# Optimization experiments

Hardware: AMD Instinct MI355X
Metric: run time of the kernel (lower is better)

Reference implementation:

```python
import jax, jax.numpy as jnp
import numpy as np

C = 1.0          # ball curvature magnitude (manifold.c)
EPS = 1e-5       # boundary projection epsilon
MIN_NORM = 1e-15

def _norm(x):
    return jnp.maximum(jnp.linalg.norm(x, axis=-1, keepdims=True), MIN_NORM)

def artanh(x):
    return jnp.arctanh(jnp.clip(x, -1.0 + 1e-7, 1.0 - 1e-7))

def proj(x, c=C):
    # clip points to the open Poincare ball of radius 1/sqrt(c)
    n = _norm(x)
    maxnorm = (1.0 - EPS) / jnp.sqrt(c)
    return jnp.where(n > maxnorm, x / n * maxnorm, x)

def logmap0(x, c=C):
    sc = jnp.sqrt(c)
    n = _norm(x)
    return artanh(sc * n) * x / (sc * n)

def expmap0(u, c=C):
    sc = jnp.sqrt(c)
    n = _norm(u)
    return jnp.tanh(sc * n) * u / (sc * n)

def gyro_add(x, y, c=C):
    # Mobius (gyrovector) addition
    x2 = jnp.sum(x * x, -1, keepdims=True)
    y2 = jnp.sum(y * y, -1, keepdims=True)
    xy = jnp.sum(x * y, -1, keepdims=True)
    num = (1.0 + 2.0 * c * xy + c * y2) * x + (1.0 - c * x2) * y
    den = 1.0 + 2.0 * c * xy + c * c * x2 * y2
    return num / jnp.maximum(den, MIN_NORM)

def gyro_matvec(W, x, c=C):
    # Mobius matrix-vector multiplication (pv_gyro_matvec)
    sc = jnp.sqrt(c)
    xn = _norm(x)
    mx = x @ W.T                       # [N, out]
    mxn = _norm(mx)
    res = jnp.tanh(mxn / xn * artanh(sc * xn)) * mx / (mxn * sc)
    zero = jnp.all(mx == 0.0, axis=-1, keepdims=True)
    return jnp.where(zero, jnp.zeros_like(res), res)

def hyp_linear(x, W, b, c=C):
    # CustomHyperbolicLinear (activation=None branch): mobius matvec + hyp bias gyro-add
    res = proj(gyro_matvec(W, x, c), c)
    hyp_bias = proj(expmap0(b[None, :], c), c)   # proj_tan0 is identity on the ball
    res = proj(gyro_add(res, hyp_bias, c), c)
    return res

def hyp_tanh_act(x, c=C):
    # CustomHyperbolicActivation(manifold, nn.Tanh()): tanh in tangent space at origin
    x = proj(x, c)
    t = jnp.tanh(logmap0(x, c))
    return proj(expmap0(t, c), c)


def setup_inputs() -> dict:
    key = jax.random.key(0)
    k0, k1, k2 = jax.random.split(key, 3)
    N, D, H = 32768, 1024, 1024
    x = proj(0.1 * jax.random.normal(k0, (N, D), dtype=jnp.float32))
    gain = float(np.sqrt(2.0))
    bound1 = gain * float(np.sqrt(6.0 / (D + H)))   # xavier_uniform with gain sqrt(2)
    W1 = jax.random.uniform(k1, (H, D), jnp.float32, -bound1, bound1)
    b1 = jnp.zeros((H,), jnp.float32)
    bound2 = gain * float(np.sqrt(6.0 / (H + H)))
    W2 = jax.random.uniform(k2, (H, H), jnp.float32, -bound2, bound2)
    b2 = jnp.zeros((H,), jnp.float32)
    return {"x": x, "W1": W1, "b1": b1, "W2": W2, "b2": b2}


def reference(x, W1, b1, W2, b2):
    # GeometricModel forward: two CustomHyperbolicLayer blocks
    # (hyperbolic linear -> tangent-space tanh activation)
    h = hyp_linear(x, W1, b1)
    h = hyp_tanh_act(h)
    h = hyp_linear(h, W2, b2)
    h = hyp_tanh_act(h)
    return h
```

## Files before the change

### kernel.cpp

```cpp
#include <hip/hip_runtime.h>


typedef short short8 __attribute__((ext_vector_type(8)));
typedef unsigned short u16x8 __attribute__((ext_vector_type(8)));
typedef unsigned short u16x4 __attribute__((ext_vector_type(4)));
typedef float f32x4 __attribute__((ext_vector_type(4)));

#define MAXN (1.0f - 1e-5f)

__device__ __forceinline__ float bf2f(unsigned short u) {
    return __uint_as_float(((unsigned int)u) << 16);
}
__device__ __forceinline__ unsigned short f2bf(float f) {
    unsigned int u = __float_as_uint(f);
    u += 0x7FFFu + ((u >> 16) & 1u);
    return (unsigned short)(u >> 16);
}
__device__ __forceinline__ float wave_sum(float v) {
#pragma unroll
    for (int m = 32; m > 0; m >>= 1) v += __shfl_xor(v, m, 64);
    return v;
}
__device__ __forceinline__ float tanh_fast(float x) {
    float e = __expf(2.0f * x);
    return 1.0f - __fdividef(2.0f, e + 1.0f);
}
__device__ __forceinline__ float artanh_clip(float x) {
    x = fminf(fmaxf(x, -1.0f + 1e-7f), 1.0f - 1e-7f);
    return 0.5f * __logf(__fdividef(1.0f + x, 1.0f - x));
}

__device__ __forceinline__ void gld_lds16(const unsigned short* g, unsigned short* l) {
    __builtin_amdgcn_global_load_lds(
        (const __attribute__((address_space(1))) unsigned int*)g,
        (__attribute__((address_space(3))) unsigned int*)l,
        16, 0, 0);
}

__global__ __launch_bounds__(256) void cast_x_kernel(
    const float* __restrict__ X, unsigned short* __restrict__ Xb,
    float* __restrict__ xn, int K)
{
    int row = blockIdx.x * 4 + (threadIdx.x >> 6);
    int l = threadIdx.x & 63;
    const float4* xr = (const float4*)(X + (size_t)row * K);
    u16x4* xw = (u16x4*)(Xb + (size_t)row * K);
    float ss = 0.f;
#pragma unroll
    for (int i = 0; i < 4; ++i) {
        float4 v = xr[i * 64 + l];
        ss += v.x * v.x + v.y * v.y + v.z * v.z + v.w * v.w;
        u16x4 o;
        o[0] = f2bf(v.x); o[1] = f2bf(v.y); o[2] = f2bf(v.z); o[3] = f2bf(v.w);
        xw[i * 64 + l] = o;
    }
    ss = wave_sum(ss);
    if (l == 0) xn[row] = fmaxf(sqrtf(ss), 1e-15f);
}

__global__ __launch_bounds__(256) void cast_w_kernel(
    const float* __restrict__ W1, unsigned short* __restrict__ W1b,
    const float* __restrict__ W2, unsigned short* __restrict__ W2b, int n4each)
{
    int i = blockIdx.x * 256 + threadIdx.x;
    const float4* src;
    u16x4* dst;
    if (i < n4each) { src = (const float4*)W1; dst = (u16x4*)W1b; }
    else            { src = (const float4*)W2; dst = (u16x4*)W2b; i -= n4each; }
    float4 v = src[i];
    u16x4 o;
    o[0] = f2bf(v.x); o[1] = f2bf(v.y); o[2] = f2bf(v.z); o[3] = f2bf(v.w);
    dst[i] = o;
}

#define STAGE(rs_, kt_) do {                                            \
    const int ko_ = (kt_) << 5;                                         \
    gld_lds16(Ab + ga0 + ko_, &sA[(rs_) * 8192 + c0 * 8]);              \
    gld_lds16(Ab + ga1 + ko_, &sA[(rs_) * 8192 + c1 * 8]);              \
    gld_lds16(Bb + ga0 + ko_, &sB[(rs_) * 8192 + c0 * 8]);              \
    gld_lds16(Bb + ga1 + ko_, &sB[(rs_) * 8192 + c1 * 8]);              \
} while (0)

#define LDFRAG(FA_, FB_, kt_) do {                                                  \
    const int rb_ = ((kt_) & 3) * 8192;                                             \
    const unsigned short* pa_ = &sA[rb_ + (wm + lr) * 32 + swo];                    \
    const unsigned short* pb_ = &sB[rb_ + (wn + lr) * 32 + swo];                    \
    _Pragma("unroll")                                                               \
    for (int m_ = 0; m_ < 8; ++m_) FA_[m_] = *(const short8*)(pa_ + m_ * 512);      \
    _Pragma("unroll")                                                               \
    for (int n_ = 0; n_ < 4; ++n_) FB_[n_] = *(const short8*)(pb_ + n_ * 512);      \
} while (0)

#define MFMAB(FA_, FB_)                                                             \
    _Pragma("unroll")                                                               \
    for (int m_ = 0; m_ < 8; ++m_)                                                  \
        _Pragma("unroll")                                                           \
        for (int n_ = 0; n_ < 4; ++n_)                                              \
            acc[m_][n_] = __builtin_amdgcn_mfma_f32_16x16x32_bf16(                  \
                FA_[m_], FB_[n_], acc[m_][n_], 0, 0, 0);

#define PSTEP(kt_, FAC_, FBC_, FAN_, FBN_, DOSTAGE_, DOPF_, DOVM_, VMSTR_, DOBAR_) {\
    if (DOSTAGE_) { STAGE((((kt_) + 3) & 3), (kt_) + 3); }                          \
    if (DOPF_) { LDFRAG(FAN_, FBN_, (kt_) + 1); }                                   \
    __builtin_amdgcn_s_setprio(1);                                                  \
    MFMAB(FAC_, FBC_);                                                              \
    __builtin_amdgcn_s_setprio(0);                                                  \
    if (DOVM_) { asm volatile("s_waitcnt vmcnt(" VMSTR_ ")" ::: "memory"); }        \
    if (DOBAR_) { __builtin_amdgcn_s_barrier(); }                                   \
}

__global__ __launch_bounds__(512, 2) void gemm_bt_kernel(
    const unsigned short* __restrict__ A,
    const unsigned short* __restrict__ B,
    unsigned short* __restrict__ C,
    int M, int Nc, int K)
{
    __shared__ __align__(16) unsigned short sA[4 * 256 * 32];
    __shared__ __align__(16) unsigned short sB[4 * 256 * 32];

    const int t = threadIdx.x;
    const int l = t & 63;
    const int w = t >> 6;
    const int lr = l & 15;
    const int lq = l >> 4;

    const int nwg = gridDim.x;
    const int cpx = nwg >> 3;
    const int swz = (blockIdx.x & 7) * cpx + (blockIdx.x >> 3);
    const int nb = Nc >> 8;
    const int bm = swz / nb;
    const int bn = swz % nb;

    const unsigned short* Ab = A + (size_t)bm * 256 * K;
    const unsigned short* Bb = B + (size_t)bn * 256 * K;

    const int wm = (w >> 2) * 128;
    const int wn = (w & 3) * 64;

    const int c0 = t, c1 = t + 512;
    const int r0 = c0 >> 2, s0 = (c0 & 3) ^ ((r0 >> 1) & 3);
    const int r1 = c1 >> 2, s1 = (c1 & 3) ^ ((r1 >> 1) & 3);
    const size_t ga0 = (size_t)r0 * K + s0 * 8;
    const size_t ga1 = (size_t)r1 * K + s1 * 8;

    const int swo = (lq ^ ((lr >> 1) & 3)) * 8;

    f32x4 acc[8][4];
#pragma unroll
    for (int i = 0; i < 8; ++i)
#pragma unroll
        for (int j = 0; j < 4; ++j)
            acc[i][j] = (f32x4){0.f, 0.f, 0.f, 0.f};

    STAGE(0, 0);
    STAGE(1, 1);
    STAGE(2, 2);
    asm volatile("s_waitcnt vmcnt(4)" ::: "memory");
    __builtin_amdgcn_s_barrier();

    short8 fa0[8], fb0[4], fa1[8], fb1[4];
    LDFRAG(fa0, fb0, 0);

    const int NTK = K >> 5;
    int kt = 0;
#pragma unroll 1
    for (; kt < NTK - 4; kt += 2) {
        PSTEP(kt,     fa0, fb0, fa1, fb1, true, true, true, "4", true);
        PSTEP(kt + 1, fa1, fb1, fa0, fb0, true, true, true, "4", true);
    }
    PSTEP(NTK - 4, fa0, fb0, fa1, fb1, true,  true,  true,  "4", true);
    PSTEP(NTK - 3, fa1, fb1, fa0, fb0, false, true,  true,  "0", true);
    PSTEP(NTK - 2, fa0, fb0, fa1, fb1, false, true,  false, "0", false);
    PSTEP(NTK - 1, fa1, fb1, fa0, fb0, false, false, false, "0", false);

    unsigned short* Cb = C + (size_t)(bm * 256 + wm) * Nc + bn * 256 + wn;
#pragma unroll
    for (int i = 0; i < 8; ++i)
#pragma unroll
        for (int r = 0; r < 4; ++r) {
            unsigned short* Cr = Cb + (size_t)(i * 16 + lq * 4 + r) * Nc + lr;
#pragma unroll
            for (int j = 0; j < 4; ++j)
                Cr[j * 16] = f2bf(acc[i][j][r]);
        }
}

template <int OUTF32>
__global__ __launch_bounds__(256) void hyp_epilogue_kernel(
    const unsigned short* __restrict__ mx, const float* __restrict__ xn_in,
    const float* __restrict__ bvec, void* __restrict__ outp,
    float* __restrict__ xn_out, int H)
{
    int row = blockIdx.x * 4 + (threadIdx.x >> 6);
    int l = threadIdx.x & 63;
    const u16x8* mrow = (const u16x8*)(mx + (size_t)row * H);
    u16x8 mv0 = mrow[l], mv1 = mrow[64 + l];
    const float4* bf4 = (const float4*)bvec;
    float4 bq0 = bf4[l * 2], bq1 = bf4[l * 2 + 1];
    float4 bq2 = bf4[128 + l * 2], bq3 = bf4[128 + l * 2 + 1];

    float m[16], b[16];
#pragma unroll
    for (int i = 0; i < 8; ++i) { m[i] = bf2f(mv0[i]); m[8 + i] = bf2f(mv1[i]); }
    b[0] = bq0.x; b[1] = bq0.y; b[2] = bq0.z; b[3] = bq0.w;
    b[4] = bq1.x; b[5] = bq1.y; b[6] = bq1.z; b[7] = bq1.w;
    b[8] = bq2.x; b[9] = bq2.y; b[10] = bq2.z; b[11] = bq2.w;
    b[12] = bq3.x; b[13] = bq3.y; b[14] = bq3.z; b[15] = bq3.w;

    float ssm = 0.f, ssb = 0.f, dmb = 0.f;
#pragma unroll
    for (int i = 0; i < 16; ++i) {
        ssm += m[i] * m[i]; ssb += b[i] * b[i]; dmb += m[i] * b[i];
    }
    ssm = wave_sum(ssm); ssb = wave_sum(ssb); dmb = wave_sum(dmb);

    float mxn = fmaxf(sqrtf(ssm), 1e-15f);
    float bn  = fmaxf(sqrtf(ssb), 1e-15f);
    float xn  = xn_in[row];

    float tt = tanh_fast(__fdividef(mxn, xn) * artanh_clip(xn));
    float rnorm = fabsf(tt);
    float pr = (rnorm > MAXN) ? __fdividef(MAXN, rnorm) : 1.0f;
    float resScale = __fdividef(tt * pr, mxn);
    float rn = fminf(rnorm, MAXN);
    float x2 = rn * rn;

    float tb = tanh_fast(bn);
    float hbn = fabsf(tb);
    float pb = (hbn > MAXN) ? __fdividef(MAXN, hbn) : 1.0f;
    float hscale = __fdividef(tb, bn) * pb;
    float hn = fminf(hbn, MAXN);
    float y2 = hn * hn;

    float xy = resScale * hscale * dmb;
    float ca = 1.0f + 2.0f * xy + y2;
    float cb = 1.0f - x2;
    float den = fmaxf(1.0f + 2.0f * xy + x2 * y2, 1e-15f);
    float fA = __fdividef(ca * resScale, den);
    float fB = __fdividef(cb * hscale, den);

    float ssz = fA * fA * ssm + 2.0f * fA * fB * dmb + fB * fB * ssb;
    float zn = fmaxf(sqrtf(fmaxf(ssz, 0.0f)), 1e-15f);
    float pz = (zn > MAXN) ? __fdividef(MAXN, zn) : 1.0f;
    float n2 = fmaxf(fminf(zn, MAXN), 1e-15f);
    float g = __fdividef(artanh_clip(n2), n2) * pz;

    float u[16];
    float ssu = 0.f;
#pragma unroll
    for (int i = 0; i < 16; ++i) {
        float zi = fA * m[i] + fB * b[i];
        u[i] = tanh_fast(g * zi);
        ssu += u[i] * u[i];
    }
    ssu = wave_sum(ssu);
    float un = fmaxf(sqrtf(ssu), 1e-15f);
    float te = tanh_fast(un);
    float on = fabsf(te);
    float po = (on > MAXN) ? __fdividef(MAXN, on) : 1.0f;
    float os = __fdividef(te, un) * po;

    if (OUTF32) {
        float* of = (float*)outp + (size_t)row * H;
        float4* of4 = (float4*)of;
        float4 a0, a1, a2, a3;
        a0.x = os * u[0];  a0.y = os * u[1];  a0.z = os * u[2];  a0.w = os * u[3];
        a1.x = os * u[4];  a1.y = os * u[5];  a1.z = os * u[6];  a1.w = os * u[7];
        a2.x = os * u[8];  a2.y = os * u[9];  a2.z = os * u[10]; a2.w = os * u[11];
        a3.x = os * u[12]; a3.y = os * u[13]; a3.z = os * u[14]; a3.w = os * u[15];
        of4[l * 2] = a0; of4[l * 2 + 1] = a1;
        of4[128 + l * 2] = a2; of4[128 + l * 2 + 1] = a3;
    } else {
        u16x8 o0, o1;
#pragma unroll
        for (int i = 0; i < 8; ++i) { o0[i] = f2bf(os * u[i]); o1[i] = f2bf(os * u[8 + i]); }
        u16x8* orow = (u16x8*)((unsigned short*)outp + (size_t)row * H);
        orow[l] = o0; orow[64 + l] = o1;
    }
    if (l == 0) xn_out[row] = fmaxf(fminf(on, MAXN), 1e-15f);
}

extern "C" void kernel_launch(void* const* d_in, const int* in_sizes, int n_in,
                              void* d_out, int out_size, void* d_ws, size_t ws_size,
                              hipStream_t stream)
{
    const float* x  = (const float*)d_in[0];
    const float* W1 = (const float*)d_in[1];
    const float* b1 = (const float*)d_in[2];
    const float* W2 = (const float*)d_in[3];
    const float* b2 = (const float*)d_in[4];

    const int H = in_sizes[2];
    const int D = in_sizes[1] / H;
    const int N = in_sizes[0] / D;

    unsigned short* stage = (unsigned short*)d_out;
    float* outf = (float*)d_out;

    unsigned short* mxb = (unsigned short*)d_ws;
    unsigned short* W1b = mxb + (size_t)N * H;
    unsigned short* W2b = W1b + (size_t)H * D;
    float* xn1 = (float*)(W2b + (size_t)H * H);
    float* xn2 = xn1 + N;

    dim3 blk(256);
    dim3 gblk(512);
    const int gemm_grid = (N / 256) * (H / 256);
    const int n4w = H * D / 4;

    cast_x_kernel<<<N / 4, blk, 0, stream>>>(x, stage, xn1, D);
    cast_w_kernel<<<(2 * n4w + 255) / 256, blk, 0, stream>>>(W1, W1b, W2, W2b, n4w);
    gemm_bt_kernel<<<gemm_grid, gblk, 0, stream>>>(stage, W1b, mxb, N, H, D);
    hyp_epilogue_kernel<0><<<N / 4, blk, 0, stream>>>(mxb, xn1, b1, stage, xn2, H);
    gemm_bt_kernel<<<gemm_grid, gblk, 0, stream>>>(stage, W2b, mxb, N, H, H);
    hyp_epilogue_kernel<1><<<N / 4, blk, 0, stream>>>(mxb, xn2, b2, outf, xn1, H);
}
```

Before: 470.1 us.

## Shrink GEMM tile to 128x128 with 3-slot LDS ring and 256-thread blocks

The bf16 GEMM drops from 256x256 tiles with 512 threads and a 4-deep LDS ring to 128x128 tiles with 256 threads, a 3-slot LDS ring and launch bounds allowing 3 blocks per CU. The main loop is unrolled by 6 to cycle the ring slots statically, and an lgkmcnt wait now precedes each barrier. The aim is more resident blocks and better latency hiding across many more workgroups. In exchange each tile reuses its global loads less, so memory traffic per flop rises.

Result: slower. 487.2 us (+3.6%).

```diff
diff --git a/kernel.cpp b/kernel.cpp
--- a/kernel.cpp
+++ b/kernel.cpp
@@ -73,50 +73,54 @@
     dst[i] = o;
 }
 
-#define STAGE(rs_, kt_) do {                                            \
+#define VMC(n_) asm volatile("s_waitcnt vmcnt(" #n_ ")" ::: "memory")
+
+#define STAGE3(slot_, kt_) do {                                         \
     const int ko_ = (kt_) << 5;                                         \
-    gld_lds16(Ab + ga0 + ko_, &sA[(rs_) * 8192 + c0 * 8]);              \
-    gld_lds16(Ab + ga1 + ko_, &sA[(rs_) * 8192 + c1 * 8]);              \
-    gld_lds16(Bb + ga0 + ko_, &sB[(rs_) * 8192 + c0 * 8]);              \
-    gld_lds16(Bb + ga1 + ko_, &sB[(rs_) * 8192 + c1 * 8]);              \
+    gld_lds16(Ab + ga0 + ko_, &sA[(slot_) * 4096 + c0 * 8]);            \
+    gld_lds16(Ab + ga1 + ko_, &sA[(slot_) * 4096 + c1 * 8]);            \
+    gld_lds16(Bb + ga0 + ko_, &sB[(slot_) * 4096 + c0 * 8]);            \
+    gld_lds16(Bb + ga1 + ko_, &sB[(slot_) * 4096 + c1 * 8]);            \
 } while (0)
 
-#define LDFRAG(FA_, FB_, kt_) do {                                                  \
-    const int rb_ = ((kt_) & 3) * 8192;                                             \
-    const unsigned short* pa_ = &sA[rb_ + (wm + lr) * 32 + swo];                    \
-    const unsigned short* pb_ = &sB[rb_ + (wn + lr) * 32 + swo];                    \
+#define LDFRAG3(FA_, FB_, slot_) do {                                               \
+    const unsigned short* pa_ = &sA[(slot_) * 4096 + (wm + lr) * 32 + swo];         \
+    const unsigned short* pb_ = &sB[(slot_) * 4096 + (wn + lr) * 32 + swo];         \
     _Pragma("unroll")                                                               \
-    for (int m_ = 0; m_ < 8; ++m_) FA_[m_] = *(const short8*)(pa_ + m_ * 512);      \
+    for (int m_ = 0; m_ < 4; ++m_) FA_[m_] = *(const short8*)(pa_ + m_ * 512);      \
     _Pragma("unroll")                                                               \
     for (int n_ = 0; n_ < 4; ++n_) FB_[n_] = *(const short8*)(pb_ + n_ * 512);      \
 } while (0)
 
-#define MFMAB(FA_, FB_)                                                             \
+#define MFMAB3(FA_, FB_)                                                            \
     _Pragma("unroll")                                                               \
-    for (int m_ = 0; m_ < 8; ++m_)                                                  \
+    for (int m_ = 0; m_ < 4; ++m_)                                                  \
         _Pragma("unroll")                                                           \
         for (int n_ = 0; n_ < 4; ++n_)                                              \
             acc[m_][n_] = __builtin_amdgcn_mfma_f32_16x16x32_bf16(                  \
                 FA_[m_], FB_[n_], acc[m_][n_], 0, 0, 0);
 
-#define PSTEP(kt_, FAC_, FBC_, FAN_, FBN_, DOSTAGE_, DOPF_, DOVM_, VMSTR_, DOBAR_) {\
-    if (DOSTAGE_) { STAGE((((kt_) + 3) & 3), (kt_) + 3); }                          \
-    if (DOPF_) { LDFRAG(FAN_, FBN_, (kt_) + 1); }                                   \
+#define PS3(KT_, SLST_, SLPF_, FAC_, FBC_, FAN_, FBN_, DOST_, DOPF_, DOVM_, VMS_, DOBAR_) { \
+    if (DOST_) { STAGE3(SLST_, (KT_) + 3); }                                        \
+    if (DOPF_) { LDFRAG3(FAN_, FBN_, SLPF_); }                                      \
     __builtin_amdgcn_s_setprio(1);                                                  \
-    MFMAB(FAC_, FBC_);                                                              \
+    MFMAB3(FAC_, FBC_);                                                             \
     __builtin_amdgcn_s_setprio(0);                                                  \
-    if (DOVM_) { asm volatile("s_waitcnt vmcnt(" VMSTR_ ")" ::: "memory"); }        \
-    if (DOBAR_) { __builtin_amdgcn_s_barrier(); }                                   \
-}
-
-__global__ __launch_bounds__(512, 2) void gemm_bt_kernel(
+    if (DOVM_) { asm volatile("s_waitcnt vmcnt(" VMS_ ")" ::: "memory"); }          \
+    if (DOBAR_) {                                                                   \
+        asm volatile("s_waitcnt lgkmcnt(0)" ::: "memory");                          \
+        __builtin_amdgcn_s_barrier();                                               \
+    }                                                                               \
+}
+
+__global__ __launch_bounds__(256, 3) void gemm_bt_kernel(
     const unsigned short* __restrict__ A,
     const unsigned short* __restrict__ B,
     unsigned short* __restrict__ C,
     int M, int Nc, int K)
 {
-    __shared__ __align__(16) unsigned short sA[4 * 256 * 32];
-    __shared__ __align__(16) unsigned short sB[4 * 256 * 32];
+    __shared__ __align__(16) unsigned short sA[3 * 128 * 32];
+    __shared__ __align__(16) unsigned short sB[3 * 128 * 32];
 
     const int t = threadIdx.x;
     const int l = t & 63;
@@ -127,17 +131,17 @@
     const int nwg = gridDim.x;
     const int cpx = nwg >> 3;
     const int swz = (blockIdx.x & 7) * cpx + (blockIdx.x >> 3);
-    const int nb = Nc >> 8;
+    const int nb = Nc >> 7;
     const int bm = swz / nb;
     const int bn = swz % nb;
 
-    const unsigned short* Ab = A + (size_t)bm * 256 * K;
-    const unsigned short* Bb = B + (size_t)bn * 256 * K;
-
-    const int wm = (w >> 2) * 128;
-    const int wn = (w & 3) * 64;
-
-    const int c0 = t, c1 = t + 512;
+    const unsigned short* Ab = A + (size_t)bm * 128 * K;
+    const unsigned short* Bb = B + (size_t)bn * 128 * K;
+
+    const int wm = (w >> 1) * 64;
+    const int wn = (w & 1) * 64;
+
+    const int c0 = t, c1 = t + 256;
     const int r0 = c0 >> 2, s0 = (c0 & 3) ^ ((r0 >> 1) & 3);
     const int r1 = c1 >> 2, s1 = (c1 & 3) ^ ((r1 >> 1) & 3);
     const size_t ga0 = (size_t)r0 * K + s0 * 8;
@@ -145,37 +149,47 @@
 
     const int swo = (lq ^ ((lr >> 1) & 3)) * 8;
 
-    f32x4 acc[8][4];
-#pragma unroll
-    for (int i = 0; i < 8; ++i)
+    f32x4 acc[4][4];
+#pragma unroll
+    for (int i = 0; i < 4; ++i)
 #pragma unroll
         for (int j = 0; j < 4; ++j)
             acc[i][j] = (f32x4){0.f, 0.f, 0.f, 0.f};
 
-    STAGE(0, 0);
-    STAGE(1, 1);
-    STAGE(2, 2);
-    asm volatile("s_waitcnt vmcnt(4)" ::: "memory");
+    STAGE3(0, 0);
+    STAGE3(1, 1);
+    STAGE3(2, 2);
+    VMC(4);
     __builtin_amdgcn_s_barrier();
 
-    short8 fa0[8], fb0[4], fa1[8], fb1[4];
-    LDFRAG(fa0, fb0, 0);
+    short8 fa0[4], fb0[4], fa1[4], fb1[4];
+    LDFRAG3(fa0, fb0, 0);
+    asm volatile("s_waitcnt lgkmcnt(0)" ::: "memory");
+    __builtin_amdgcn_s_barrier();
 
     const int NTK = K >> 5;
     int kt = 0;
 #pragma unroll 1
-    for (; kt < NTK - 4; kt += 2) {
-        PSTEP(kt,     fa0, fb0, fa1, fb1, true, true, true, "4", true);
-        PSTEP(kt + 1, fa1, fb1, fa0, fb0, true, true, true, "4", true);
-    }
-    PSTEP(NTK - 4, fa0, fb0, fa1, fb1, true,  true,  true,  "4", true);
-    PSTEP(NTK - 3, fa1, fb1, fa0, fb0, false, true,  true,  "0", true);
-    PSTEP(NTK - 2, fa0, fb0, fa1, fb1, false, true,  false, "0", false);
-    PSTEP(NTK - 1, fa1, fb1, fa0, fb0, false, false, false, "0", false);
-
-    unsigned short* Cb = C + (size_t)(bm * 256 + wm) * Nc + bn * 256 + wn;
-#pragma unroll
-    for (int i = 0; i < 8; ++i)
+    for (; kt < NTK - 8; kt += 6) {
+        PS3(kt,     0, 1, fa0, fb0, fa1, fb1, 1, 1, 1, "4", 1);
+        PS3(kt + 1, 1, 2, fa1, fb1, fa0, fb0, 1, 1, 1, "4", 1);
+        PS3(kt + 2, 2, 0, fa0, fb0, fa1, fb1, 1, 1, 1, "4", 1);
+        PS3(kt + 3, 0, 1, fa1, fb1, fa0, fb0, 1, 1, 1, "4", 1);
+        PS3(kt + 4, 1, 2, fa0, fb0, fa1, fb1, 1, 1, 1, "4", 1);
+        PS3(kt + 5, 2, 0, fa1, fb1, fa0, fb0, 1, 1, 1, "4", 1);
+    }
+    PS3(NTK - 8, 0, 1, fa0, fb0, fa1, fb1, 1, 1, 1, "4", 1);
+    PS3(NTK - 7, 1, 2, fa1, fb1, fa0, fb0, 1, 1, 1, "4", 1);
+    PS3(NTK - 6, 2, 0, fa0, fb0, fa1, fb1, 1, 1, 1, "4", 1);
+    PS3(NTK - 5, 0, 1, fa1, fb1, fa0, fb0, 1, 1, 1, "4", 1);
+    PS3(NTK - 4, 1, 2, fa0, fb0, fa1, fb1, 1, 1, 1, "4", 1);
+    PS3(NTK - 3, 2, 0, fa1, fb1, fa0, fb0, 0, 1, 1, "0", 1);
+    PS3(NTK - 2, 0, 1, fa0, fb0, fa1, fb1, 0, 1, 0, "0", 0);
+    PS3(NTK - 1, 0, 0, fa1, fb1, fa0, fb0, 0, 0, 0, "0", 0);
+
+    unsigned short* Cb = C + (size_t)(bm * 128 + wm) * Nc + bn * 128 + wn;
+#pragma unroll
+    for (int i = 0; i < 4; ++i)
 #pragma unroll
         for (int r = 0; r < 4; ++r) {
             unsigned short* Cr = Cb + (size_t)(i * 16 + lq * 4 + r) * Nc + lr;
@@ -304,14 +318,13 @@
     float* xn2 = xn1 + N;
 
     dim3 blk(256);
-    dim3 gblk(512);
-    const int gemm_grid = (N / 256) * (H / 256);
+    const int gemm_grid = (N / 128) * (H / 128);
     const int n4w = H * D / 4;
 
     cast_x_kernel<<<N / 4, blk, 0, stream>>>(x, stage, xn1, D);
     cast_w_kernel<<<(2 * n4w + 255) / 256, blk, 0, stream>>>(W1, W1b, W2, W2b, n4w);
-    gemm_bt_kernel<<<gemm_grid, gblk, 0, stream>>>(stage, W1b, mxb, N, H, D);
+    gemm_bt_kernel<<<gemm_grid, blk, 0, stream>>>(stage, W1b, mxb, N, H, D);
     hyp_epilogue_kernel<0><<<N / 4, blk, 0, stream>>>(mxb, xn1, b1, stage, xn2, H);
-    gemm_bt_kernel<<<gemm_grid, gblk, 0, stream>>>(stage, W2b, mxb, N, H, H);
+    gemm_bt_kernel<<<gemm_grid, blk, 0, stream>>>(stage, W2b, mxb, N, H, H);
     hyp_epilogue_kernel<1><<<N / 4, blk, 0, stream>>>(mxb, xn2, b2, outf, xn1, H);
 }
```

## Fuse x cast, GEMM and hyperbolic epilogue into one full-row layer kernel

Applied to the files above, without the earlier changes.

Replaces the separate cast, 256x256-tile GEMM and row epilogue kernels with one kernel per layer. Each block owns 64 full output rows across all 1024 columns, so row norms and dot products can be reduced in-block and the bf16 intermediate mx never goes to global memory. The first layer also converts x to bf16 and computes its norm while staging. In exchange the tile is narrow (64 rows), the pipeline drops from 4-stage to 2-stage double buffering with a full wait every step, and occupancy is one block per CU with a large LDS footprint. Together these may lower MFMA efficiency relative to the earlier tuned GEMM.

After: 507.3 us. 1.08x slower.

```diff
diff --git a/kernel.cpp b/kernel.cpp
--- a/kernel.cpp
+++ b/kernel.cpp
@@ -35,27 +35,6 @@
         (const __attribute__((address_space(1))) unsigned int*)g,
         (__attribute__((address_space(3))) unsigned int*)l,
         16, 0, 0);
-}
-
-__global__ __launch_bounds__(256) void cast_x_kernel(
-    const float* __restrict__ X, unsigned short* __restrict__ Xb,
-    float* __restrict__ xn, int K)
-{
-    int row = blockIdx.x * 4 + (threadIdx.x >> 6);
-    int l = threadIdx.x & 63;
-    const float4* xr = (const float4*)(X + (size_t)row * K);
-    u16x4* xw = (u16x4*)(Xb + (size_t)row * K);
-    float ss = 0.f;
-#pragma unroll
-    for (int i = 0; i < 4; ++i) {
-        float4 v = xr[i * 64 + l];
-        ss += v.x * v.x + v.y * v.y + v.z * v.z + v.w * v.w;
-        u16x4 o;
-        o[0] = f2bf(v.x); o[1] = f2bf(v.y); o[2] = f2bf(v.z); o[3] = f2bf(v.w);
-        xw[i * 64 + l] = o;
-    }
-    ss = wave_sum(ss);
-    if (l == 0) xn[row] = fmaxf(sqrtf(ss), 1e-15f);
 }
 
 __global__ __launch_bounds__(256) void cast_w_kernel(
@@ -73,150 +52,163 @@
     dst[i] = o;
 }
 
-#define STAGE(rs_, kt_) do {                                            \
-    const int ko_ = (kt_) << 5;                                         \
-    gld_lds16(Ab + ga0 + ko_, &sA[(rs_) * 8192 + c0 * 8]);              \
-    gld_lds16(Ab + ga1 + ko_, &sA[(rs_) * 8192 + c1 * 8]);              \
-    gld_lds16(Bb + ga0 + ko_, &sB[(rs_) * 8192 + c0 * 8]);              \
-    gld_lds16(Bb + ga1 + ko_, &sB[(rs_) * 8192 + c1 * 8]);              \
-} while (0)
-
-#define LDFRAG(FA_, FB_, kt_) do {                                                  \
-    const int rb_ = ((kt_) & 3) * 8192;                                             \
-    const unsigned short* pa_ = &sA[rb_ + (wm + lr) * 32 + swo];                    \
-    const unsigned short* pb_ = &sB[rb_ + (wn + lr) * 32 + swo];                    \
-    _Pragma("unroll")                                                               \
-    for (int m_ = 0; m_ < 8; ++m_) FA_[m_] = *(const short8*)(pa_ + m_ * 512);      \
-    _Pragma("unroll")                                                               \
-    for (int n_ = 0; n_ < 4; ++n_) FB_[n_] = *(const short8*)(pb_ + n_ * 512);      \
-} while (0)
-
-#define MFMAB(FA_, FB_)                                                             \
-    _Pragma("unroll")                                                               \
-    for (int m_ = 0; m_ < 8; ++m_)                                                  \
-        _Pragma("unroll")                                                           \
-        for (int n_ = 0; n_ < 4; ++n_)                                              \
-            acc[m_][n_] = __builtin_amdgcn_mfma_f32_16x16x32_bf16(                  \
-                FA_[m_], FB_[n_], acc[m_][n_], 0, 0, 0);
-
-#define PSTEP(kt_, FAC_, FBC_, FAN_, FBN_, DOSTAGE_, DOPF_, DOVM_, VMSTR_, DOBAR_) {\
-    if (DOSTAGE_) { STAGE((((kt_) + 3) & 3), (kt_) + 3); }                          \
-    if (DOPF_) { LDFRAG(FAN_, FBN_, (kt_) + 1); }                                   \
-    __builtin_amdgcn_s_setprio(1);                                                  \
-    MFMAB(FAC_, FBC_);                                                              \
-    __builtin_amdgcn_s_setprio(0);                                                  \
-    if (DOVM_) { asm volatile("s_waitcnt vmcnt(" VMSTR_ ")" ::: "memory"); }        \
-    if (DOBAR_) { __builtin_amdgcn_s_barrier(); }                                   \
-}
-
-__global__ __launch_bounds__(512, 2) void gemm_bt_kernel(
-    const unsigned short* __restrict__ A,
+template <int FIRST>
+__global__ __launch_bounds__(512, 1) void fused_layer_kernel(
+    const float* __restrict__ Af,
+    const unsigned short* __restrict__ Ah,
     const unsigned short* __restrict__ B,
-    unsigned short* __restrict__ C,
-    int M, int Nc, int K)
+    const float* __restrict__ bvec,
+    const float* __restrict__ xn_in,
+    void* __restrict__ outp,
+    float* __restrict__ xn_out,
+    int K, int Nc)
 {
-    __shared__ __align__(16) unsigned short sA[4 * 256 * 32];
-    __shared__ __align__(16) unsigned short sB[4 * 256 * 32];
+    __shared__ __align__(16) unsigned short sB[2][1024 * 32];
+    __shared__ __align__(16) unsigned short sA[2][64 * 32];
+    __shared__ __align__(16) float sP1[64 * 8];
+    __shared__ __align__(16) float sP2[64 * 8];
+    __shared__ __align__(16) float sF[64 * 4];
+    __shared__ __align__(16) float sXN[64];
 
     const int t = threadIdx.x;
     const int l = t & 63;
     const int w = t >> 6;
     const int lr = l & 15;
     const int lq = l >> 4;
-
-    const int nwg = gridDim.x;
-    const int cpx = nwg >> 3;
-    const int swz = (blockIdx.x & 7) * cpx + (blockIdx.x >> 3);
-    const int nb = Nc >> 8;
-    const int bm = swz / nb;
-    const int bn = swz % nb;
-
-    const unsigned short* Ab = A + (size_t)bm * 256 * K;
-    const unsigned short* Bb = B + (size_t)bn * 256 * K;
-
-    const int wm = (w >> 2) * 128;
-    const int wn = (w & 3) * 64;
-
-    const int c0 = t, c1 = t + 512;
-    const int r0 = c0 >> 2, s0 = (c0 & 3) ^ ((r0 >> 1) & 3);
-    const int r1 = c1 >> 2, s1 = (c1 & 3) ^ ((r1 >> 1) & 3);
-    const size_t ga0 = (size_t)r0 * K + s0 * 8;
-    const size_t ga1 = (size_t)r1 * K + s1 * 8;
+    const int g0 = blockIdx.x * 64;
+    const int wn = w * 128;
+
+    size_t gaB[8];
+    int ldB[8];
+#pragma unroll
+    for (int j = 0; j < 8; ++j) {
+        int c = t + 512 * j;
+        int r = c >> 2, s = (c & 3) ^ ((r >> 1) & 3);
+        gaB[j] = (size_t)r * K + s * 8;
+        ldB[j] = c * 8;
+    }
+    const int rA = t >> 2;
+    const int sAs = (t & 3) ^ ((rA >> 1) & 3);
+    const size_t gaA = (size_t)(g0 + rA) * K + sAs * 8;
 
     const int swo = (lq ^ ((lr >> 1) & 3)) * 8;
 
-    f32x4 acc[8][4];
-#pragma unroll
-    for (int i = 0; i < 8; ++i)
-#pragma unroll
-        for (int j = 0; j < 4; ++j)
-            acc[i][j] = (f32x4){0.f, 0.f, 0.f, 0.f};
-
-    STAGE(0, 0);
-    STAGE(1, 1);
-    STAGE(2, 2);
-    asm volatile("s_waitcnt vmcnt(4)" ::: "memory");
+    f32x4 acc[4][8];
+#pragma unroll
+    for (int m = 0; m < 4; ++m)
+#pragma unroll
+        for (int n = 0; n < 8; ++n)
+            acc[m][n] = (f32x4){0.f, 0.f, 0.f, 0.f};
+
+    float ss = 0.f;
+
+    auto stage = [&](int buf, int kt) {
+#pragma unroll
+        for (int j = 0; j < 8; ++j)
+            gld_lds16(B + gaB[j] + kt * 32, &sB[buf][ldB[j]]);
+        if (t < 256) {
+            if constexpr (FIRST) {
+                float4 v0 = *(const float4*)(Af + gaA + kt * 32);
+                float4 v1 = *(const float4*)(Af + gaA + kt * 32 + 4);
+                ss += v0.x * v0.x + v0.y * v0.y + v0.z * v0.z + v0.w * v0.w;
+                ss += v1.x * v1.x + v1.y * v1.y + v1.z * v1.z + v1.w * v1.w;
+                u16x8 o;
+                o[0] = f2bf(v0.x); o[1] = f2bf(v0.y); o[2] = f2bf(v0.z); o[3] = f2bf(v0.w);
+                o[4] = f2bf(v1.x); o[5] = f2bf(v1.y); o[6] = f2bf(v1.z); o[7] = f2bf(v1.w);
+                *(u16x8*)&sA[buf][t * 8] = o;
+            } else {
+                gld_lds16(Ah + gaA + kt * 32, &sA[buf][t * 8]);
+            }
+        }
+    };
+
+    stage(0, 0);
+    asm volatile("s_waitcnt vmcnt(0) lgkmcnt(0)" ::: "memory");
     __builtin_amdgcn_s_barrier();
 
-    short8 fa0[8], fb0[4], fa1[8], fb1[4];
-    LDFRAG(fa0, fb0, 0);
-
     const int NTK = K >> 5;
-    int kt = 0;
 #pragma unroll 1
-    for (; kt < NTK - 4; kt += 2) {
-        PSTEP(kt,     fa0, fb0, fa1, fb1, true, true, true, "4", true);
-        PSTEP(kt + 1, fa1, fb1, fa0, fb0, true, true, true, "4", true);
-    }
-    PSTEP(NTK - 4, fa0, fb0, fa1, fb1, true,  true,  true,  "4", true);
-    PSTEP(NTK - 3, fa1, fb1, fa0, fb0, false, true,  true,  "0", true);
-    PSTEP(NTK - 2, fa0, fb0, fa1, fb1, false, true,  false, "0", false);
-    PSTEP(NTK - 1, fa1, fb1, fa0, fb0, false, false, false, "0", false);
-
-    unsigned short* Cb = C + (size_t)(bm * 256 + wm) * Nc + bn * 256 + wn;
-#pragma unroll
-    for (int i = 0; i < 8; ++i)
+    for (int kt = 0; kt < NTK; ++kt) {
+        const int buf = kt & 1;
+        if (kt + 1 < NTK) stage(buf ^ 1, kt + 1);
+        short8 a[4], b[8];
+#pragma unroll
+        for (int m = 0; m < 4; ++m)
+            a[m] = *(const short8*)&sA[buf][(m * 16 + lr) * 32 + swo];
+#pragma unroll
+        for (int n = 0; n < 8; ++n)
+            b[n] = *(const short8*)&sB[buf][(wn + n * 16 + lr) * 32 + swo];
+        __builtin_amdgcn_s_setprio(1);
+#pragma unroll
+        for (int m = 0; m < 4; ++m)
+#pragma unroll
+            for (int n = 0; n < 8; ++n)
+                acc[m][n] = __builtin_amdgcn_mfma_f32_16x16x32_bf16(a[m], b[n], acc[m][n], 0, 0, 0);
+        __builtin_amdgcn_s_setprio(0);
+        asm volatile("s_waitcnt vmcnt(0) lgkmcnt(0)" ::: "memory");
+        __builtin_amdgcn_s_barrier();
+    }
+
+
+    if constexpr (FIRST) {
+        if (t < 256) {
+            float s2 = ss;
+            s2 += __shfl_xor(s2, 1, 64);
+            s2 += __shfl_xor(s2, 2, 64);
+            if ((t & 3) == 0) sXN[t >> 2] = fmaxf(sqrtf(s2), 1e-15f);
+        }
+    }
+
+    float bn_[8];
+#pragma unroll
+    for (int n = 0; n < 8; ++n) bn_[n] = bvec[wn + n * 16 + lr];
+
+    float pm[4][4], pd[4][4];
+#pragma unroll
+    for (int m = 0; m < 4; ++m)
 #pragma unroll
         for (int r = 0; r < 4; ++r) {
-            unsigned short* Cr = Cb + (size_t)(i * 16 + lq * 4 + r) * Nc + lr;
-#pragma unroll
-            for (int j = 0; j < 4; ++j)
-                Cr[j * 16] = f2bf(acc[i][j][r]);
-        }
-}
-
-template <int OUTF32>
-__global__ __launch_bounds__(256) void hyp_epilogue_kernel(
-    const unsigned short* __restrict__ mx, const float* __restrict__ xn_in,
-    const float* __restrict__ bvec, void* __restrict__ outp,
-    float* __restrict__ xn_out, int H)
-{
-    int row = blockIdx.x * 4 + (threadIdx.x >> 6);
-    int l = threadIdx.x & 63;
-    const u16x8* mrow = (const u16x8*)(mx + (size_t)row * H);
-    u16x8 mv0 = mrow[l], mv1 = mrow[64 + l];
-    const float4* bf4 = (const float4*)bvec;
-    float4 bq0 = bf4[l * 2], bq1 = bf4[l * 2 + 1];
-    float4 bq2 = bf4[128 + l * 2], bq3 = bf4[128 + l * 2 + 1];
-
-    float m[16], b[16];
-#pragma unroll
-    for (int i = 0; i < 8; ++i) { m[i] = bf2f(mv0[i]); m[8 + i] = bf2f(mv1[i]); }
-    b[0] = bq0.x; b[1] = bq0.y; b[2] = bq0.z; b[3] = bq0.w;
-    b[4] = bq1.x; b[5] = bq1.y; b[6] = bq1.z; b[7] = bq1.w;
-    b[8] = bq2.x; b[9] = bq2.y; b[10] = bq2.z; b[11] = bq2.w;
-    b[12] = bq3.x; b[13] = bq3.y; b[14] = bq3.z; b[15] = bq3.w;
-
-    float ssm = 0.f, ssb = 0.f, dmb = 0.f;
-#pragma unroll
-    for (int i = 0; i < 16; ++i) {
-        ssm += m[i] * m[i]; ssb += b[i] * b[i]; dmb += m[i] * b[i];
-    }
-    ssm = wave_sum(ssm); ssb = wave_sum(ssb); dmb = wave_sum(dmb);
-
+            float sm = 0.f, sd = 0.f;
+#pragma unroll
+            for (int n = 0; n < 8; ++n) {
+                float v = acc[m][n][r];
+                sm += v * v;
+                sd += v * bn_[n];
+            }
+            pm[m][r] = sm; pd[m][r] = sd;
+        }
+#pragma unroll
+    for (int mask = 1; mask <= 8; mask <<= 1)
+#pragma unroll
+        for (int m = 0; m < 4; ++m)
+#pragma unroll
+            for (int r = 0; r < 4; ++r) {
+                pm[m][r] += __shfl_xor(pm[m][r], mask, 64);
+                pd[m][r] += __shfl_xor(pd[m][r], mask, 64);
+            }
+    if (lr == 0) {
+#pragma unroll
+        for (int m = 0; m < 4; ++m)
+#pragma unroll
+            for (int r = 0; r < 4; ++r) {
+                int row = m * 16 + lq * 4 + r;
+                sP1[row * 8 + w] = pm[m][r];
+                sP2[row * 8 + w] = pd[m][r];
+            }
+    }
+    __syncthreads();
+
+    float ssm = 0.f, dmb = 0.f;
+#pragma unroll
+    for (int j = 0; j < 8; ++j) { ssm += sP1[l * 8 + j]; dmb += sP2[l * 8 + j]; }
+    float ssb = 0.f;
+#pragma unroll
+    for (int j = 0; j < 16; ++j) { float bj = bvec[l + 64 * j]; ssb += bj * bj; }
+    ssb = wave_sum(ssb);
+
+    float xn = FIRST ? sXN[l] : fmaxf(xn_in[g0 + l], 1e-15f);
     float mxn = fmaxf(sqrtf(ssm), 1e-15f);
-    float bn  = fmaxf(sqrtf(ssb), 1e-15f);
-    float xn  = xn_in[row];
+    float bnn = fmaxf(sqrtf(ssb), 1e-15f);
 
     float tt = tanh_fast(__fdividef(mxn, xn) * artanh_clip(xn));
     float rnorm = fabsf(tt);
@@ -224,60 +216,94 @@
     float resScale = __fdividef(tt * pr, mxn);
     float rn = fminf(rnorm, MAXN);
     float x2 = rn * rn;
-
-    float tb = tanh_fast(bn);
+    float tb = tanh_fast(bnn);
     float hbn = fabsf(tb);
     float pb = (hbn > MAXN) ? __fdividef(MAXN, hbn) : 1.0f;
-    float hscale = __fdividef(tb, bn) * pb;
+    float hscale = __fdividef(tb, bnn) * pb;
     float hn = fminf(hbn, MAXN);
     float y2 = hn * hn;
-
     float xy = resScale * hscale * dmb;
     float ca = 1.0f + 2.0f * xy + y2;
     float cb = 1.0f - x2;
     float den = fmaxf(1.0f + 2.0f * xy + x2 * y2, 1e-15f);
     float fA = __fdividef(ca * resScale, den);
     float fB = __fdividef(cb * hscale, den);
-
     float ssz = fA * fA * ssm + 2.0f * fA * fB * dmb + fB * fB * ssb;
     float zn = fmaxf(sqrtf(fmaxf(ssz, 0.0f)), 1e-15f);
     float pz = (zn > MAXN) ? __fdividef(MAXN, zn) : 1.0f;
     float n2 = fmaxf(fminf(zn, MAXN), 1e-15f);
     float g = __fdividef(artanh_clip(n2), n2) * pz;
 
-    float u[16];
+    if (w == 0) {
+        float4 f4; f4.x = fA; f4.y = fB; f4.z = g; f4.w = 0.f;
+        *(float4*)&sF[l * 4] = f4;
+    }
+    __syncthreads();
+
+    float pu[4][4];
+#pragma unroll
+    for (int m = 0; m < 4; ++m)
+#pragma unroll
+        for (int r = 0; r < 4; ++r) {
+            int row = m * 16 + lq * 4 + r;
+            float4 f = *(const float4*)&sF[row * 4];
+            float su = 0.f;
+#pragma unroll
+            for (int n = 0; n < 8; ++n) {
+                float z = f.x * acc[m][n][r] + f.y * bn_[n];
+                float u = tanh_fast(f.z * z);
+                acc[m][n][r] = u;
+                su += u * u;
+            }
+            pu[m][r] = su;
+        }
+#pragma unroll
+    for (int mask = 1; mask <= 8; mask <<= 1)
+#pragma unroll
+        for (int m = 0; m < 4; ++m)
+#pragma unroll
+            for (int r = 0; r < 4; ++r)
+                pu[m][r] += __shfl_xor(pu[m][r], mask, 64);
+    if (lr == 0) {
+#pragma unroll
+        for (int m = 0; m < 4; ++m)
+#pragma unroll
+            for (int r = 0; r < 4; ++r)
+                sP1[(m * 16 + lq * 4 + r) * 8 + w] = pu[m][r];
+    }
+    __syncthreads();
+
     float ssu = 0.f;
 #pragma unroll
-    for (int i = 0; i < 16; ++i) {
-        float zi = fA * m[i] + fB * b[i];
-        u[i] = tanh_fast(g * zi);
-        ssu += u[i] * u[i];
-    }
-    ssu = wave_sum(ssu);
+    for (int j = 0; j < 8; ++j) ssu += sP1[l * 8 + j];
     float un = fmaxf(sqrtf(ssu), 1e-15f);
     float te = tanh_fast(un);
     float on = fabsf(te);
     float po = (on > MAXN) ? __fdividef(MAXN, on) : 1.0f;
     float os = __fdividef(te, un) * po;
-
-    if (OUTF32) {
-        float* of = (float*)outp + (size_t)row * H;
-        float4* of4 = (float4*)of;
-        float4 a0, a1, a2, a3;
-        a0.x = os * u[0];  a0.y = os * u[1];  a0.z = os * u[2];  a0.w = os * u[3];
-        a1.x = os * u[4];  a1.y = os * u[5];  a1.z = os * u[6];  a1.w = os * u[7];
-        a2.x = os * u[8];  a2.y = os * u[9];  a2.z = os * u[10]; a2.w = os * u[11];
-        a3.x = os * u[12]; a3.y = os * u[13]; a3.z = os * u[14]; a3.w = os * u[15];
-        of4[l * 2] = a0; of4[l * 2 + 1] = a1;
-        of4[128 + l * 2] = a2; of4[128 + l * 2 + 1] = a3;
-    } else {
-        u16x8 o0, o1;
-#pragma unroll
-        for (int i = 0; i < 8; ++i) { o0[i] = f2bf(os * u[i]); o1[i] = f2bf(os * u[8 + i]); }
-        u16x8* orow = (u16x8*)((unsigned short*)outp + (size_t)row * H);
-        orow[l] = o0; orow[64 + l] = o1;
-    }
-    if (l == 0) xn_out[row] = fmaxf(fminf(on, MAXN), 1e-15f);
+    if (w == 0) {
+        sXN[l] = os;
+        if constexpr (FIRST)
+            xn_out[g0 + l] = fmaxf(fminf(on, MAXN), 1e-15f);
+    }
+    __syncthreads();
+
+#pragma unroll
+    for (int m = 0; m < 4; ++m)
+#pragma unroll
+        for (int r = 0; r < 4; ++r) {
+            int row = m * 16 + lq * 4 + r;
+            float osr = sXN[row];
+            if constexpr (FIRST) {
+                unsigned short* op = (unsigned short*)outp + (size_t)(g0 + row) * Nc + wn + lr;
+#pragma unroll
+                for (int n = 0; n < 8; ++n) op[n * 16] = f2bf(osr * acc[m][n][r]);
+            } else {
+                float* op = (float*)outp + (size_t)(g0 + row) * Nc + wn + lr;
+#pragma unroll
+                for (int n = 0; n < 8; ++n) op[n * 16] = osr * acc[m][n][r];
+            }
+        }
 }
 
 extern "C" void kernel_launch(void* const* d_in, const int* in_sizes, int n_in,
@@ -294,24 +320,16 @@
     const int D = in_sizes[1] / H;
     const int N = in_sizes[0] / D;
 
-    unsigned short* stage = (unsigned short*)d_out;
+    unsigned short* hb  = (unsigned short*)d_ws;
+    unsigned short* W1b = hb + (size_t)N * H;
+    unsigned short* W2b = W1b + (size_t)H * D;
+    float* xn2 = (float*)(W2b + (size_t)H * H);
     float* outf = (float*)d_out;
 
-    unsigned short* mxb = (unsigned short*)d_ws;
-    unsigned short* W1b = mxb + (size_t)N * H;
-    unsigned short* W2b = W1b + (size_t)H * D;
-    float* xn1 = (float*)(W2b + (size_t)H * H);
-    float* xn2 = xn1 + N;
-
-    dim3 blk(256);
-    dim3 gblk(512);
-    const int gemm_grid = (N / 256) * (H / 256);
     const int n4w = H * D / 4;
-
-    cast_x_kernel<<<N / 4, blk, 0, stream>>>(x, stage, xn1, D);
-    cast_w_kernel<<<(2 * n4w + 255) / 256, blk, 0, stream>>>(W1, W1b, W2, W2b, n4w);
-    gemm_bt_kernel<<<gemm_grid, gblk, 0, stream>>>(stage, W1b, mxb, N, H, D);
-    hyp_epilogue_kernel<0><<<N / 4, blk, 0, stream>>>(mxb, xn1, b1, stage, xn2, H);
-    gemm_bt_kernel<<<gemm_grid, gblk, 0, stream>>>(stage, W2b, mxb, N, H, H);
-    hyp_epilogue_kernel<1><<<N / 4, blk, 0, stream>>>(mxb, xn2, b2, outf, xn1, H);
-}
+    cast_w_kernel<<<(2 * n4w + 255) / 256, dim3(256), 0, stream>>>(W1, W1b, W2, W2b, n4w);
+    fused_layer_kernel<1><<<N / 64, dim3(512), 0, stream>>>(
+        x, nullptr, W1b, b1, nullptr, hb, xn2, D, H);
+    fused_layer_kernel<0><<<N / 64, dim3(512), 0, stream>>>(
+        nullptr, hb, W2b, b2, xn2, outf, nullptr, H, H);
+}
```
